# Kernel tuning notes

Hardware: AMD Instinct MI355X
Metric: run time of the kernel (lower is better)

## Reference

```python
import jax, jax.numpy as jnp
import numpy as np

B, T, I, H, C = 128, 512, 256, 512, 4


def setup_inputs() -> dict:
    key = jax.random.key(0)
    ks = jax.random.split(key, 11)
    s = lambda fan_in: 1.0 / np.sqrt(fan_in)
    return {
        "x": jax.random.normal(ks[0], (B, T, I), dtype=jnp.float32),
        "W_x1": jax.random.uniform(ks[1], (I, 4 * H), jnp.float32, -s(I), s(I)),
        "b_x1": jax.random.uniform(ks[2], (4 * H,), jnp.float32, -s(I), s(I)),
        "W_h1": jax.random.uniform(ks[3], (H, 4 * H), jnp.float32, -s(H), s(H)),
        "b_h1": jax.random.uniform(ks[4], (4 * H,), jnp.float32, -s(H), s(H)),
        "W_x2": jax.random.uniform(ks[5], (H, 4 * H), jnp.float32, -s(H), s(H)),
        "b_x2": jax.random.uniform(ks[6], (4 * H,), jnp.float32, -s(H), s(H)),
        "W_h2": jax.random.uniform(ks[7], (H, 4 * H), jnp.float32, -s(H), s(H)),
        "b_h2": jax.random.uniform(ks[8], (4 * H,), jnp.float32, -s(H), s(H)),
        "W_head": jax.random.uniform(ks[9], (H, C), jnp.float32, -s(H), s(H)),
        "b_head": jax.random.uniform(ks[10], (C,), jnp.float32, -s(H), s(H)),
    }


def _lstm_layer(x_proj_seq, W_h, b_h, hidden):
    """x_proj_seq: [T, B, 4H] precomputed input projection (incl. x bias).
    Returns full hidden sequence [T, B, H] and final (h, c)."""
    def step(carry, xp_t):
        h, c = carry
        gates = xp_t + h @ W_h + b_h  # [B, 4H]
        i_t, f_t, g_t, o_t = jnp.split(gates, 4, axis=-1)
        i_t = jax.nn.sigmoid(i_t)
        f_t = jax.nn.sigmoid(f_t)
        g_t = jnp.tanh(g_t)
        o_t = jax.nn.sigmoid(o_t)
        c_t = f_t * c + i_t * g_t
        h_t = o_t * jnp.tanh(c_t)
        return (h_t, c_t), h_t

    batch = x_proj_seq.shape[1]
    init = (jnp.zeros((batch, hidden), x_proj_seq.dtype),
            jnp.zeros((batch, hidden), x_proj_seq.dtype))
    (h_T, c_T), h_seq = jax.lax.scan(step, init, x_proj_seq)
    return h_seq, h_T


def reference(x, W_x1, b_x1, W_h1, b_h1, W_x2, b_x2, W_h2, b_h2, W_head, b_head):
    H_ = W_h1.shape[0]
    # Precompute input projections for all timesteps as one big GEMM per layer.
    xp1 = jnp.einsum('bti,ig->tbg', x, W_x1) + b_x1  # [T, B, 4H]
    h1_seq, _ = _lstm_layer(xp1, W_h1, b_h1, H_)      # [T, B, H]
    xp2 = jnp.einsum('tbh,hg->tbg', h1_seq, W_x2) + b_x2
    _, h2_T = _lstm_layer(xp2, W_h2, b_h2, H_)        # [B, H]
    return h2_T @ W_head + b_head                     # [B, C]
```

## Files before the change

kernel.cpp:

```cpp
#include <hip/hip_runtime.h>
#include <cstddef>

#define Bb 128
#define Tt 512
#define Ii 256
#define Hh 512
#define G4c 2048
#define BHc (Bb * Hh)
#define FSTRIDE 32

typedef float    f32x4 __attribute__((ext_vector_type(4)));
typedef _Float16 f16x8 __attribute__((ext_vector_type(8)));
typedef unsigned int u32x4 __attribute__((ext_vector_type(4)));

#define OFF_WT1 0u
#define OFF_WT2 3145728u
#define OFF_BC1 7340032u
#define OFF_BC2 7348224u
#define OFF_H1  7356416u
#define OFF_H2  7880704u
#define OFF_FLG 8142848u
#define OFF_PRG 8159232u
#define OFF_END 8159744u

__device__ __forceinline__ float sigm(float x)  { return 1.0f / (1.0f + __expf(-x)); }
__device__ __forceinline__ float tanhf_(float x){ return 1.0f - 2.0f / (1.0f + __expf(2.0f * x)); }

__device__ __forceinline__ void ld_g_f16x8_sc(f16x8& dst, const _Float16* p) {
  asm volatile("global_load_dwordx4 %0, %1, off sc0 sc1"
               : "=v"(dst) : "v"(p) : "memory");
}
__device__ __forceinline__ void ld_g_f32x4(f32x4& dst, const float* p) {
  asm volatile("global_load_dwordx4 %0, %1, off" : "=v"(dst) : "v"(p) : "memory");
}
__device__ __forceinline__ void st_g_f16_sc(_Float16* p, _Float16 v) {
  unsigned u = (unsigned)__builtin_bit_cast(unsigned short, v);
  asm volatile("global_store_short %0, %1, off sc0 sc1" :: "v"(p), "v"(u) : "memory");
}
__device__ __forceinline__ void wait_vm0() {
  asm volatile("s_waitcnt vmcnt(0)" ::: "memory");
}

__device__ __forceinline__ void pollstep(unsigned* grpL, unsigned* peer, int tid,
                                         unsigned tl, unsigned tp) {
  if (tid < 64) {
    const unsigned tgt = (tid < 32) ? tl : tp;
    const unsigned* p = (tid < 32) ? grpL + (size_t)tid * FSTRIDE : peer;
    unsigned v;
    do {
      v = __hip_atomic_load(p, __ATOMIC_RELAXED, __HIP_MEMORY_SCOPE_AGENT);
    } while (__any(v < tgt));
  }
  __syncthreads();
}

__device__ __forceinline__ void publish(unsigned* myflag, int tid, unsigned val) {
  wait_vm0();
  __syncthreads();
  if (tid == 0)
    __hip_atomic_store(myflag, val, __ATOMIC_RELAXED, __HIP_MEMORY_SCOPE_AGENT);
}

__global__ void init_weights(const float* __restrict__ Wx1, const float* __restrict__ Wh1,
                             const float* __restrict__ bx1, const float* __restrict__ bh1,
                             const float* __restrict__ Wx2, const float* __restrict__ Wh2,
                             const float* __restrict__ bx2, const float* __restrict__ bh2,
                             _Float16* __restrict__ Wt1, _Float16* __restrict__ Wt2,
                             float* __restrict__ bc1, float* __restrict__ bc2) {
  const int b = blockIdx.x;
  const int layer = b >> 11;
  const int jb = (b >> 6) & 31;
  const int ln = b & 63;
  const int t  = threadIdx.x;
  const int ks = t >> 3;
  const int i  = t & 7;
  const int k  = (ks << 5) + ((ln >> 4) << 3) + i;
  if (layer == 0) {
    if (ln == 0 && t < 16) {
      #pragma unroll
      for (int g = 0; g < 4; ++g) {
        const int gc = (g << 9) + (jb << 4) + t;
        bc1[gc] = bx1[gc] + bh1[gc];
      }
    }
    if (ks < 24) {
      #pragma unroll
      for (int g = 0; g < 4; ++g) {
        const int gc = (g << 9) + (jb << 4) + (ln & 15);
        const float v = (k < Ii) ? Wx1[k * G4c + gc] : Wh1[(k - Ii) * G4c + gc];
        Wt1[((((size_t)jb * 24 + ks) * 4 + g) * 64 + ln) * 8 + i] = (_Float16)v;
      }
    }
  } else {
    if (ln == 0 && t < 16) {
      #pragma unroll
      for (int g = 0; g < 4; ++g) {
        const int gc = (g << 9) + (jb << 4) + t;
        bc2[gc] = bx2[gc] + bh2[gc];
      }
    }
    #pragma unroll
    for (int g = 0; g < 4; ++g) {
      const int gc = (g << 9) + (jb << 4) + (ln & 15);
      const float v = (k < Hh) ? Wx2[k * G4c + gc] : Wh2[(k - Hh) * G4c + gc];
      Wt2[((((size_t)jb * 32 + ks) * 4 + g) * 64 + ln) * 8 + i] = (_Float16)v;
    }
  }
}

__global__ void zero_ws(u32x4* p, int n) {
  const int i = blockIdx.x * blockDim.x + threadIdx.x;
  if (i < n) p[i] = (u32x4){0u, 0u, 0u, 0u};
}

__global__ __launch_bounds__(256, 1) void lstm_main(
    const float* __restrict__ x,
    const _Float16* __restrict__ Wt1, const _Float16* __restrict__ Wt2,
    const float* __restrict__ bc1, const float* __restrict__ bc2,
    _Float16* h1buf, _Float16* h2buf, unsigned* flags, unsigned* prg,
    const float* __restrict__ Whead, const float* __restrict__ bhead,
    float* __restrict__ out)
{
  extern __shared__ char smem[];

  const int tid  = threadIdx.x;
  const int lane = tid & 63;
  const int wv   = tid >> 6;
  const int bid  = blockIdx.x;
  const int layer = bid >> 6;
  const int blkL  = bid & 63;
  const int jb = blkL >> 1;
  const int rh = blkL & 1;
  const int j0 = jb << 4;

  unsigned* grpL   = flags + (size_t)((rh << 6) + (layer << 5)) * FSTRIDE;
  unsigned* myflag = grpL + (size_t)jb * FSTRIDE;
  unsigned* ownp   = prg + (size_t)((rh << 1) | layer) * FSTRIDE;
  unsigned* peer   = prg + (size_t)((rh << 1) | (1 - layer)) * FSTRIDE;

  {
    const int elems16 = layer ? (131072 / 16) : (98304 / 16);
    const u32x4* src = (const u32x4*)((layer ? Wt2 : Wt1)
                                      + (size_t)jb * (layer ? 65536 : 49152));
    u32x4* dst = (u32x4*)smem;
    for (int i = tid; i < elems16; i += 256) dst[i] = src[i];
  }
  __syncthreads();

  const int c15 = lane & 15;
  const int kg  = lane >> 4;
  const int arow  = (rh << 6) + (wv << 4) + c15;
  const int wrow0 = (rh << 6) + (wv << 4) + (kg << 2);

  const float* bc = layer ? bc2 : bc1;
  const float bias0 = bc[        j0 + c15];
  const float bias1 = bc[ 512 +  j0 + c15];
  const float bias2 = bc[1024 +  j0 + c15];
  const float bias3 = bc[1536 +  j0 + c15];

  const int lb = lane << 4;

  f32x4 cst = {0.f, 0.f, 0.f, 0.f};

  for (int e = 0; e <= Tt; ++e) {
    if (layer == 0) {
      if (e >= Tt) break;
      f32x4 xf[16];
      const float* xp = x + (size_t)arow * (Tt * Ii) + (size_t)e * Ii + (kg << 3);
      #pragma unroll
      for (int ks = 0; ks < 8; ++ks) {
        ld_g_f32x4(xf[2*ks],   xp + (ks << 5));
        ld_g_f32x4(xf[2*ks+1], xp + (ks << 5) + 4);
      }
      pollstep(grpL, peer, tid, (unsigned)e, (e >= 2) ? (unsigned)(e - 2) : 0u);
      if (jb == 0 && tid == 0)
        __hip_atomic_store(ownp, (unsigned)e, __ATOMIC_RELAXED, __HIP_MEMORY_SCOPE_AGENT);
      f16x8 af[24];
      const _Float16* hp = h1buf + (size_t)((e - 1) & 3) * BHc + arow * Hh + (kg << 3);
      #pragma unroll
      for (int ks = 0; ks < 16; ++ks)
        ld_g_f16x8_sc(af[8 + ks], hp + (ks << 5));
      wait_vm0();
      __builtin_amdgcn_sched_barrier(0);
      #pragma unroll
      for (int ks = 0; ks < 8; ++ks) {
        f16x8 v;
        v[0] = (_Float16)xf[2*ks][0]; v[1] = (_Float16)xf[2*ks][1];
        v[2] = (_Float16)xf[2*ks][2]; v[3] = (_Float16)xf[2*ks][3];
        v[4] = (_Float16)xf[2*ks+1][0]; v[5] = (_Float16)xf[2*ks+1][1];
        v[6] = (_Float16)xf[2*ks+1][2]; v[7] = (_Float16)xf[2*ks+1][3];
        af[ks] = v;
      }
      f32x4 acc0 = {0.f,0.f,0.f,0.f}, acc1 = {0.f,0.f,0.f,0.f};
      f32x4 acc2 = {0.f,0.f,0.f,0.f}, acc3 = {0.f,0.f,0.f,0.f};
      #pragma unroll
      for (int ks = 0; ks < 24; ++ks) {
        const char* bp = smem + (ks << 12) + lb;
        acc0 = __builtin_amdgcn_mfma_f32_16x16x32_f16(af[ks], *(const f16x8*)(bp       ), acc0, 0, 0, 0);
        acc1 = __builtin_amdgcn_mfma_f32_16x16x32_f16(af[ks], *(const f16x8*)(bp + 1024), acc1, 0, 0, 0);
        acc2 = __builtin_amdgcn_mfma_f32_16x16x32_f16(af[ks], *(const f16x8*)(bp + 2048), acc2, 0, 0, 0);
        acc3 = __builtin_amdgcn_mfma_f32_16x16x32_f16(af[ks], *(const f16x8*)(bp + 3072), acc3, 0, 0, 0);
      }
      float hout[4];
      #pragma unroll
      for (int r = 0; r < 4; ++r) {
        const float iv = sigm(acc0[r] + bias0);
        const float fv = sigm(acc1[r] + bias1);
        const float gv = tanhf_(acc2[r] + bias2);
        const float ov = sigm(acc3[r] + bias3);
        const float cv = fv * cst[r] + iv * gv;
        cst[r] = cv;
        hout[r] = ov * tanhf_(cv);
      }
      _Float16* hw = h1buf + (size_t)(e & 3) * BHc;
      #pragma unroll
      for (int r = 0; r < 4; ++r)
        st_g_f16_sc(hw + (size_t)(wrow0 + r) * Hh + j0 + c15, (_Float16)hout[r]);
      publish(myflag, tid, (unsigned)(e + 1));
    } else {
      if (e == 0) {
        publish(myflag, tid, 1u);
      } else {
        pollstep(grpL, peer, tid, (unsigned)e, (unsigned)e);
        if (jb == 0 && tid == 0)
          __hip_atomic_store(ownp, (unsigned)e, __ATOMIC_RELAXED, __HIP_MEMORY_SCOPE_AGENT);
        f16x8 af[32];
        const _Float16* h1p = h1buf + (size_t)((e - 1) & 3) * BHc + arow * Hh + (kg << 3);
        const _Float16* h2p = h2buf + (size_t)(e & 1) * BHc + arow * Hh + (kg << 3);
        #pragma unroll
        for (int ks = 0; ks < 16; ++ks)
          ld_g_f16x8_sc(af[ks], h1p + (ks << 5));
        #pragma unroll
        for (int ks = 0; ks < 16; ++ks)
          ld_g_f16x8_sc(af[16 + ks], h2p + (ks << 5));
        wait_vm0();
        __builtin_amdgcn_sched_barrier(0);
        f32x4 acc0 = {0.f,0.f,0.f,0.f}, acc1 = {0.f,0.f,0.f,0.f};
        f32x4 acc2 = {0.f,0.f,0.f,0.f}, acc3 = {0.f,0.f,0.f,0.f};
        #pragma unroll
        for (int ks = 0; ks < 32; ++ks) {
          const char* bp = smem + (ks << 12) + lb;
          acc0 = __builtin_amdgcn_mfma_f32_16x16x32_f16(af[ks], *(const f16x8*)(bp       ), acc0, 0, 0, 0);
          acc1 = __builtin_amdgcn_mfma_f32_16x16x32_f16(af[ks], *(const f16x8*)(bp + 1024), acc1, 0, 0, 0);
          acc2 = __builtin_amdgcn_mfma_f32_16x16x32_f16(af[ks], *(const f16x8*)(bp + 2048), acc2, 0, 0, 0);
          acc3 = __builtin_amdgcn_mfma_f32_16x16x32_f16(af[ks], *(const f16x8*)(bp + 3072), acc3, 0, 0, 0);
        }
        float hout[4];
        #pragma unroll
        for (int r = 0; r < 4; ++r) {
          const float iv = sigm(acc0[r] + bias0);
          const float fv = sigm(acc1[r] + bias1);
          const float gv = tanhf_(acc2[r] + bias2);
          const float ov = sigm(acc3[r] + bias3);
          const float cv = fv * cst[r] + iv * gv;
          cst[r] = cv;
          hout[r] = ov * tanhf_(cv);
        }
        _Float16* hw = h2buf + (size_t)((e + 1) & 1) * BHc;
        #pragma unroll
        for (int r = 0; r < 4; ++r)
          st_g_f16_sc(hw + (size_t)(wrow0 + r) * Hh + j0 + c15, (_Float16)hout[r]);
        publish(myflag, tid, (unsigned)(e + 1));
      }
    }
  }

  if (layer == 0) {
    if (jb == 0) {
      pollstep(grpL, peer, tid, (unsigned)Tt, 0u);
      if (tid == 0)
        __hip_atomic_store(ownp, (unsigned)Tt, __ATOMIC_RELAXED, __HIP_MEMORY_SCOPE_AGENT);
    }
  } else if (jb == 0) {
    pollstep(grpL, peer, tid, (unsigned)(Tt + 1), 0u);
    const int b_ = (rh << 6) + (tid >> 2);
    const int cc = tid & 3;
    const _Float16* hr = h2buf + BHc + (size_t)b_ * Hh;
    float s = bhead[cc];
    #pragma unroll
    for (int half = 0; half < 2; ++half) {
      f16x8 hv[32];
      #pragma unroll
      for (int kk = 0; kk < 32; ++kk)
        ld_g_f16x8_sc(hv[kk], hr + (half << 8) + (kk << 3));
      wait_vm0();
      #pragma unroll
      for (int kk = 0; kk < 32; ++kk) {
        const int k = (half << 8) + (kk << 3);
        #pragma unroll
        for (int j = 0; j < 8; ++j)
          s += (float)hv[kk][j] * Whead[(k + j) * 4 + cc];
      }
    }
    out[b_ * 4 + cc] = s;
  }
}

extern "C" void kernel_launch(void* const* d_in, const int* in_sizes, int n_in,
                              void* d_out, int out_size, void* d_ws, size_t ws_size,
                              hipStream_t stream) {
  const float* x   = (const float*)d_in[0];
  const float* Wx1 = (const float*)d_in[1];
  const float* bx1 = (const float*)d_in[2];
  const float* Wh1 = (const float*)d_in[3];
  const float* bh1 = (const float*)d_in[4];
  const float* Wx2 = (const float*)d_in[5];
  const float* bx2 = (const float*)d_in[6];
  const float* Wh2 = (const float*)d_in[7];
  const float* bh2 = (const float*)d_in[8];
  const float* Whd = (const float*)d_in[9];
  const float* bhd = (const float*)d_in[10];

  char* ws = (char*)d_ws;
  _Float16* Wt1 = (_Float16*)(ws + OFF_WT1);
  _Float16* Wt2 = (_Float16*)(ws + OFF_WT2);
  float* bc1 = (float*)(ws + OFF_BC1);
  float* bc2 = (float*)(ws + OFF_BC2);
  _Float16* h1b = (_Float16*)(ws + OFF_H1);
  _Float16* h2b = (_Float16*)(ws + OFF_H2);
  unsigned* flg = (unsigned*)(ws + OFF_FLG);
  unsigned* prg = (unsigned*)(ws + OFF_PRG);
  float* out = (float*)d_out;

  init_weights<<<4096, 256, 0, stream>>>(Wx1, Wh1, bx1, bh1, Wx2, Wh2, bx2, bh2,
                                         Wt1, Wt2, bc1, bc2);
  {
    u32x4* zp = (u32x4*)(ws + OFF_H1);
    const int n = (int)((OFF_END - OFF_H1) / 16);
    zero_ws<<<(n + 255) / 256, 256, 0, stream>>>(zp, n);
  }
  (void)hipFuncSetAttribute((const void*)lstm_main,
                            hipFuncAttributeMaxDynamicSharedMemorySize, 131072);
  void* args[] = {(void*)&x, (void*)&Wt1, (void*)&Wt2, (void*)&bc1, (void*)&bc2,
                  (void*)&h1b, (void*)&h2b, (void*)&flg, (void*)&prg,
                  (void*)&Whd, (void*)&bhd, (void*)&out};
  (void)hipLaunchCooperativeKernel((const void*)lstm_main, dim3(128), dim3(256),
                                   args, 131072, stream);
}
```

Measured before the change: 4.045 ms.

## Pack per-group flags into one cache line and vectorize hidden-state stores via LDS transpose

Each group's 32 per-block progress flags now sit contiguously in one cache line instead of being padded 128 bytes apart, so the polling wavefront reads one line rather than 32. The gate accumulators are also staged through a shared-memory buffer and remapped so each thread computes 4 contiguous hidden units and writes them with a single 8-byte store instead of four 2-byte scattered stores. The cost is an extra LDS round trip plus a __syncthreads per step, and possible false sharing when 32 blocks write atomics to the same flag line.

```diff
diff --git a/kernel.cpp b/kernel.cpp
--- a/kernel.cpp
+++ b/kernel.cpp
@@ -7,10 +7,10 @@
 #define Hh 512
 #define G4c 2048
 #define BHc (Bb * Hh)
-#define FSTRIDE 32
 
 typedef float    f32x4 __attribute__((ext_vector_type(4)));
 typedef _Float16 f16x8 __attribute__((ext_vector_type(8)));
+typedef unsigned int u32x2 __attribute__((ext_vector_type(2)));
 typedef unsigned int u32x4 __attribute__((ext_vector_type(4)));
 
 #define OFF_WT1 0u
@@ -20,8 +20,8 @@
 #define OFF_H1  7356416u
 #define OFF_H2  7880704u
 #define OFF_FLG 8142848u
-#define OFF_PRG 8159232u
-#define OFF_END 8159744u
+#define OFF_PRG 8143360u
+#define OFF_END 8143872u
 
 __device__ __forceinline__ float sigm(float x)  { return 1.0f / (1.0f + __expf(-x)); }
 __device__ __forceinline__ float tanhf_(float x){ return 1.0f - 2.0f / (1.0f + __expf(2.0f * x)); }
@@ -33,19 +33,23 @@
 __device__ __forceinline__ void ld_g_f32x4(f32x4& dst, const float* p) {
   asm volatile("global_load_dwordx4 %0, %1, off" : "=v"(dst) : "v"(p) : "memory");
 }
-__device__ __forceinline__ void st_g_f16_sc(_Float16* p, _Float16 v) {
-  unsigned u = (unsigned)__builtin_bit_cast(unsigned short, v);
-  asm volatile("global_store_short %0, %1, off sc0 sc1" :: "v"(p), "v"(u) : "memory");
+__device__ __forceinline__ void st_g_u32x2_sc(void* p, u32x2 v) {
+  asm volatile("global_store_dwordx2 %0, %1, off sc0 sc1" :: "v"(p), "v"(v) : "memory");
 }
 __device__ __forceinline__ void wait_vm0() {
   asm volatile("s_waitcnt vmcnt(0)" ::: "memory");
 }
-
-__device__ __forceinline__ void pollstep(unsigned* grpL, unsigned* peer, int tid,
+__device__ __forceinline__ unsigned packh(float a, float b) {
+  unsigned short ua = __builtin_bit_cast(unsigned short, (_Float16)a);
+  unsigned short ub = __builtin_bit_cast(unsigned short, (_Float16)b);
+  return (unsigned)ua | ((unsigned)ub << 16);
+}
+
+__device__ __forceinline__ void pollstep(unsigned* ownline, unsigned* peer, int tid,
                                          unsigned tl, unsigned tp) {
   if (tid < 64) {
     const unsigned tgt = (tid < 32) ? tl : tp;
-    const unsigned* p = (tid < 32) ? grpL + (size_t)tid * FSTRIDE : peer;
+    const unsigned* p = (tid < 32) ? ownline + tid : peer;
     unsigned v;
     do {
       v = __hip_atomic_load(p, __ATOMIC_RELAXED, __HIP_MEMORY_SCOPE_AGENT);
@@ -54,11 +58,11 @@
   __syncthreads();
 }
 
-__device__ __forceinline__ void publish(unsigned* myflag, int tid, unsigned val) {
+__device__ __forceinline__ void publish(unsigned* myword, int tid, unsigned val) {
   wait_vm0();
   __syncthreads();
   if (tid == 0)
-    __hip_atomic_store(myflag, val, __ATOMIC_RELAXED, __HIP_MEMORY_SCOPE_AGENT);
+    __hip_atomic_store(myword, val, __ATOMIC_RELAXED, __HIP_MEMORY_SCOPE_AGENT);
 }
 
 __global__ void init_weights(const float* __restrict__ Wx1, const float* __restrict__ Wh1,
@@ -122,6 +126,7 @@
     float* __restrict__ out)
 {
   extern __shared__ char smem[];
+  __shared__ f32x4 gxs[1024];
 
   const int tid  = threadIdx.x;
   const int lane = tid & 63;
@@ -132,11 +137,12 @@
   const int jb = blkL >> 1;
   const int rh = blkL & 1;
   const int j0 = jb << 4;
-
-  unsigned* grpL   = flags + (size_t)((rh << 6) + (layer << 5)) * FSTRIDE;
-  unsigned* myflag = grpL + (size_t)jb * FSTRIDE;
-  unsigned* ownp   = prg + (size_t)((rh << 1) | layer) * FSTRIDE;
-  unsigned* peer   = prg + (size_t)((rh << 1) | (1 - layer)) * FSTRIDE;
+  const int g4 = (rh << 1) | layer;
+
+  unsigned* ownline = flags + (size_t)g4 * 32;
+  unsigned* myword  = ownline + jb;
+  unsigned* ownp    = prg + (size_t)g4 * 32;
+  unsigned* peer    = prg + (size_t)((rh << 1) | (1 - layer)) * 32;
 
   {
     const int elems16 = layer ? (131072 / 16) : (98304 / 16);
@@ -149,14 +155,17 @@
 
   const int c15 = lane & 15;
   const int kg  = lane >> 4;
-  const int arow  = (rh << 6) + (wv << 4) + c15;
-  const int wrow0 = (rh << 6) + (wv << 4) + (kg << 2);
-
-  const float* bc = layer ? bc2 : bc1;
-  const float bias0 = bc[        j0 + c15];
-  const float bias1 = bc[ 512 +  j0 + c15];
-  const float bias2 = bc[1024 +  j0 + c15];
-  const float bias3 = bc[1536 +  j0 + c15];
+  const int arow = (rh << 6) + (wv << 4) + c15;
+
+  const int rr = tid >> 2;
+  const int qq = tid & 3;
+  const int wv_r = rr >> 4, kg_r = (rr >> 2) & 3, r_r = rr & 3;
+  const float* bcL = layer ? bc2 : bc1;
+  f32x4 bi0 = *(const f32x4*)(bcL +        j0 + (qq << 2));
+  f32x4 bi1 = *(const f32x4*)(bcL +  512 + j0 + (qq << 2));
+  f32x4 bi2 = *(const f32x4*)(bcL + 1024 + j0 + (qq << 2));
+  f32x4 bi3 = *(const f32x4*)(bcL + 1536 + j0 + (qq << 2));
+  const size_t eoff = (size_t)((rh << 6) + rr) * Hh + j0 + (qq << 2);
 
   const int lb = lane << 4;
 
@@ -172,7 +181,7 @@
         ld_g_f32x4(xf[2*ks],   xp + (ks << 5));
         ld_g_f32x4(xf[2*ks+1], xp + (ks << 5) + 4);
       }
-      pollstep(grpL, peer, tid, (unsigned)e, (e >= 2) ? (unsigned)(e - 2) : 0u);
+      pollstep(ownline, peer, tid, (unsigned)e, (e >= 2) ? (unsigned)(e - 2) : 0u);
       if (jb == 0 && tid == 0)
         __hip_atomic_store(ownp, (unsigned)e, __ATOMIC_RELAXED, __HIP_MEMORY_SCOPE_AGENT);
       f16x8 af[24];
@@ -201,27 +210,32 @@
         acc2 = __builtin_amdgcn_mfma_f32_16x16x32_f16(af[ks], *(const f16x8*)(bp + 2048), acc2, 0, 0, 0);
         acc3 = __builtin_amdgcn_mfma_f32_16x16x32_f16(af[ks], *(const f16x8*)(bp + 3072), acc3, 0, 0, 0);
       }
-      float hout[4];
-      #pragma unroll
-      for (int r = 0; r < 4; ++r) {
-        const float iv = sigm(acc0[r] + bias0);
-        const float fv = sigm(acc1[r] + bias1);
-        const float gv = tanhf_(acc2[r] + bias2);
-        const float ov = sigm(acc3[r] + bias3);
-        const float cv = fv * cst[r] + iv * gv;
-        cst[r] = cv;
-        hout[r] = ov * tanhf_(cv);
-      }
-      _Float16* hw = h1buf + (size_t)(e & 3) * BHc;
-      #pragma unroll
-      for (int r = 0; r < 4; ++r)
-        st_g_f16_sc(hw + (size_t)(wrow0 + r) * Hh + j0 + c15, (_Float16)hout[r]);
-      publish(myflag, tid, (unsigned)(e + 1));
+      gxs[((wv*4 + 0)*16 + c15)*4 + kg] = acc0;
+      gxs[((wv*4 + 1)*16 + c15)*4 + kg] = acc1;
+      gxs[((wv*4 + 2)*16 + c15)*4 + kg] = acc2;
+      gxs[((wv*4 + 3)*16 + c15)*4 + kg] = acc3;
+      __syncthreads();
+      const float* gb = (const float*)gxs;
+      float hv[4];
+      #pragma unroll
+      for (int cc = 0; cc < 4; ++cc) {
+        const int fi = (wv_r*4)*256 + ((qq<<2) + cc)*16 + (kg_r<<2) + r_r;
+        const float iv = sigm (gb[fi      ] + bi0[cc]);
+        const float fv = sigm (gb[fi + 256] + bi1[cc]);
+        const float gv = tanhf_(gb[fi + 512] + bi2[cc]);
+        const float ov = sigm (gb[fi + 768] + bi3[cc]);
+        const float cv = fv * cst[cc] + iv * gv;
+        cst[cc] = cv;
+        hv[cc] = ov * tanhf_(cv);
+      }
+      u32x2 pk = { packh(hv[0], hv[1]), packh(hv[2], hv[3]) };
+      st_g_u32x2_sc((char*)(h1buf + (size_t)(e & 3) * BHc + eoff), pk);
+      publish(myword, tid, (unsigned)(e + 1));
     } else {
       if (e == 0) {
-        publish(myflag, tid, 1u);
+        publish(myword, tid, 1u);
       } else {
-        pollstep(grpL, peer, tid, (unsigned)e, (unsigned)e);
+        pollstep(ownline, peer, tid, (unsigned)e, (unsigned)e);
         if (jb == 0 && tid == 0)
           __hip_atomic_store(ownp, (unsigned)e, __ATOMIC_RELAXED, __HIP_MEMORY_SCOPE_AGENT);
         f16x8 af[32];
@@ -245,34 +259,39 @@
           acc2 = __builtin_amdgcn_mfma_f32_16x16x32_f16(af[ks], *(const f16x8*)(bp + 2048), acc2, 0, 0, 0);
           acc3 = __builtin_amdgcn_mfma_f32_16x16x32_f16(af[ks], *(const f16x8*)(bp + 3072), acc3, 0, 0, 0);
         }
-        float hout[4];
-        #pragma unroll
-        for (int r = 0; r < 4; ++r) {
-          const float iv = sigm(acc0[r] + bias0);
-          const float fv = sigm(acc1[r] + bias1);
-          const float gv = tanhf_(acc2[r] + bias2);
-          const float ov = sigm(acc3[r] + bias3);
-          const float cv = fv * cst[r] + iv * gv;
-          cst[r] = cv;
-          hout[r] = ov * tanhf_(cv);
+        gxs[((wv*4 + 0)*16 + c15)*4 + kg] = acc0;
+        gxs[((wv*4 + 1)*16 + c15)*4 + kg] = acc1;
+        gxs[((wv*4 + 2)*16 + c15)*4 + kg] = acc2;
+        gxs[((wv*4 + 3)*16 + c15)*4 + kg] = acc3;
+        __syncthreads();
+        const float* gb = (const float*)gxs;
+        float hv[4];
+        #pragma unroll
+        for (int cc = 0; cc < 4; ++cc) {
+          const int fi = (wv_r*4)*256 + ((qq<<2) + cc)*16 + (kg_r<<2) + r_r;
+          const float iv = sigm (gb[fi      ] + bi0[cc]);
+          const float fv = sigm (gb[fi + 256] + bi1[cc]);
+          const float gv = tanhf_(gb[fi + 512] + bi2[cc]);
+          const float ov = sigm (gb[fi + 768] + bi3[cc]);
+          const float cv = fv * cst[cc] + iv * gv;
+          cst[cc] = cv;
+          hv[cc] = ov * tanhf_(cv);
         }
-        _Float16* hw = h2buf + (size_t)((e + 1) & 1) * BHc;
-        #pragma unroll
-        for (int r = 0; r < 4; ++r)
-          st_g_f16_sc(hw + (size_t)(wrow0 + r) * Hh + j0 + c15, (_Float16)hout[r]);
-        publish(myflag, tid, (unsigned)(e + 1));
+        u32x2 pk = { packh(hv[0], hv[1]), packh(hv[2], hv[3]) };
+        st_g_u32x2_sc((char*)(h2buf + (size_t)((e + 1) & 1) * BHc + eoff), pk);
+        publish(myword, tid, (unsigned)(e + 1));
       }
     }
   }
 
   if (layer == 0) {
     if (jb == 0) {
-      pollstep(grpL, peer, tid, (unsigned)Tt, 0u);
+      pollstep(ownline, peer, tid, (unsigned)Tt, 0u);
       if (tid == 0)
         __hip_atomic_store(ownp, (unsigned)Tt, __ATOMIC_RELAXED, __HIP_MEMORY_SCOPE_AGENT);
     }
   } else if (jb == 0) {
-    pollstep(grpL, peer, tid, (unsigned)(Tt + 1), 0u);
+    pollstep(ownline, peer, tid, (unsigned)(Tt + 1), 0u);
     const int b_ = (rh << 6) + (tid >> 2);
     const int cc = tid & 3;
     const _Float16* hr = h2buf + BHc + (size_t)b_ * Hh;
```

Result: slower. 4.281 ms (+5.8%).

## Split step barrier into half-group polls and defer peer-layer wait

Applied to the files above, without the earlier changes.

Replaces the single combined poll on all 32 group flags plus the peer-layer progress counter with finer-grained waits. The kernel first waits on the first 16 flag slots and issues loads for the first half of the recurrent h slice, then waits on the second 16 and loads the rest. The cross-layer dependency wait is moved later: for layer 0 it sits just before writing h1 into the ring buffer, and for layer 1 just before loading h1. The aim is to overlap global loads with waiting on slower blocks and to keep cross-layer waits off the critical path. The cost is extra __syncthreads and polling rounds per timestep, and a more delicate ordering argument for correctness.

```diff
diff --git a/kernel.cpp b/kernel.cpp
--- a/kernel.cpp
+++ b/kernel.cpp
@@ -39,6 +39,29 @@
 }
 __device__ __forceinline__ void wait_vm0() {
   asm volatile("s_waitcnt vmcnt(0)" ::: "memory");
+}
+
+__device__ __forceinline__ void poll_half(unsigned* base16, int tid, unsigned tgt) {
+  if (tid < 64) {
+    unsigned v = 0xffffffffu;
+    do {
+      if (tid < 16)
+        v = __hip_atomic_load(base16 + (size_t)tid * FSTRIDE,
+                              __ATOMIC_RELAXED, __HIP_MEMORY_SCOPE_AGENT);
+    } while (__any(v < tgt));
+  }
+  __syncthreads();
+}
+
+__device__ __forceinline__ void poll_peer(unsigned* peer, int tid, unsigned tgt) {
+  if (tid < 64) {
+    unsigned v = 0xffffffffu;
+    do {
+      if (tid == 0)
+        v = __hip_atomic_load(peer, __ATOMIC_RELAXED, __HIP_MEMORY_SCOPE_AGENT);
+    } while (__any(v < tgt));
+  }
+  __syncthreads();
 }
 
 __device__ __forceinline__ void pollstep(unsigned* grpL, unsigned* peer, int tid,
@@ -134,6 +157,7 @@
   const int j0 = jb << 4;
 
   unsigned* grpL   = flags + (size_t)((rh << 6) + (layer << 5)) * FSTRIDE;
+  unsigned* grpH   = grpL + (size_t)16 * FSTRIDE;
   unsigned* myflag = grpL + (size_t)jb * FSTRIDE;
   unsigned* ownp   = prg + (size_t)((rh << 1) | layer) * FSTRIDE;
   unsigned* peer   = prg + (size_t)((rh << 1) | (1 - layer)) * FSTRIDE;
@@ -172,14 +196,18 @@
         ld_g_f32x4(xf[2*ks],   xp + (ks << 5));
         ld_g_f32x4(xf[2*ks+1], xp + (ks << 5) + 4);
       }
-      pollstep(grpL, peer, tid, (unsigned)e, (e >= 2) ? (unsigned)(e - 2) : 0u);
+      f16x8 af[24];
+      const _Float16* hp = h1buf + (size_t)((e - 1) & 3) * BHc + arow * Hh + (kg << 3);
+      poll_half(grpL, tid, (unsigned)e);
+      #pragma unroll
+      for (int ks = 0; ks < 8; ++ks)
+        ld_g_f16x8_sc(af[8 + ks], hp + (ks << 5));
+      poll_half(grpH, tid, (unsigned)e);
+      #pragma unroll
+      for (int ks = 8; ks < 16; ++ks)
+        ld_g_f16x8_sc(af[8 + ks], hp + (ks << 5));
       if (jb == 0 && tid == 0)
         __hip_atomic_store(ownp, (unsigned)e, __ATOMIC_RELAXED, __HIP_MEMORY_SCOPE_AGENT);
-      f16x8 af[24];
-      const _Float16* hp = h1buf + (size_t)((e - 1) & 3) * BHc + arow * Hh + (kg << 3);
-      #pragma unroll
-      for (int ks = 0; ks < 16; ++ks)
-        ld_g_f16x8_sc(af[8 + ks], hp + (ks << 5));
       wait_vm0();
       __builtin_amdgcn_sched_barrier(0);
       #pragma unroll
@@ -212,6 +240,7 @@
         cst[r] = cv;
         hout[r] = ov * tanhf_(cv);
       }
+      poll_peer(peer, tid, (e >= 2) ? (unsigned)(e - 2) : 0u);
       _Float16* hw = h1buf + (size_t)(e & 3) * BHc;
       #pragma unroll
       for (int r = 0; r < 4; ++r)
@@ -221,18 +250,23 @@
       if (e == 0) {
         publish(myflag, tid, 1u);
       } else {
-        pollstep(grpL, peer, tid, (unsigned)e, (unsigned)e);
+        f16x8 af[32];
+        const _Float16* h2p = h2buf + (size_t)(e & 1) * BHc + arow * Hh + (kg << 3);
+        const _Float16* h1p = h1buf + (size_t)((e - 1) & 3) * BHc + arow * Hh + (kg << 3);
+        poll_half(grpL, tid, (unsigned)e);
+        #pragma unroll
+        for (int ks = 0; ks < 8; ++ks)
+          ld_g_f16x8_sc(af[16 + ks], h2p + (ks << 5));
+        poll_half(grpH, tid, (unsigned)e);
+        #pragma unroll
+        for (int ks = 8; ks < 16; ++ks)
+          ld_g_f16x8_sc(af[16 + ks], h2p + (ks << 5));
         if (jb == 0 && tid == 0)
           __hip_atomic_store(ownp, (unsigned)e, __ATOMIC_RELAXED, __HIP_MEMORY_SCOPE_AGENT);
-        f16x8 af[32];
-        const _Float16* h1p = h1buf + (size_t)((e - 1) & 3) * BHc + arow * Hh + (kg << 3);
-        const _Float16* h2p = h2buf + (size_t)(e & 1) * BHc + arow * Hh + (kg << 3);
+        poll_peer(peer, tid, (unsigned)e);
         #pragma unroll
         for (int ks = 0; ks < 16; ++ks)
           ld_g_f16x8_sc(af[ks], h1p + (ks << 5));
-        #pragma unroll
-        for (int ks = 0; ks < 16; ++ks)
-          ld_g_f16x8_sc(af[16 + ks], h2p + (ks << 5));
         wait_vm0();
         __builtin_amdgcn_sched_barrier(0);
         f32x4 acc0 = {0.f,0.f,0.f,0.f}, acc1 = {0.f,0.f,0.f,0.f};
```

Measured after the change: 4.217 ms. 4.3% more time.
